# Optimization experiments

Measured on AMD Instinct MI355X. Metric: run time of the kernel, lower is better.

Reference implementation:

```python
import jax, jax.numpy as jnp
import numpy as np

SIGMA = 1.0
RADIUS = 3          # Gaussian kernel radius -> kernel size 7
TAU = 1.0
ITERATIONS = 20
EPS = 1e-6


def _gauss_kernel_1d(sigma: float, radius: int) -> jnp.ndarray:
    x = jnp.arange(-radius, radius + 1, dtype=jnp.float32)
    k = jnp.exp(-0.5 * (x / sigma) ** 2)
    return k / k.sum()


def _smooth(v: jnp.ndarray, k1d: jnp.ndarray) -> jnp.ndarray:
    """Separable Gaussian smoothing of a (1, C, D, H, W) field, 'same' padding."""
    C = v.shape[1]
    r = (k1d.size - 1) // 2
    for ax in range(3):
        shape = [1, 1, 1]
        shape[ax] = k1d.size
        ker = jnp.tile(k1d.reshape((1, 1) + tuple(shape)), (C, 1, 1, 1, 1))
        pad = [(r, r) if i == ax else (0, 0) for i in range(3)]
        v = jax.lax.conv_general_dilated(
            v, ker, window_strides=(1, 1, 1), padding=pad,
            dimension_numbers=('NCDHW', 'OIDHW', 'NCDHW'),
            feature_group_count=C)
    return v


def _warp(image: jnp.ndarray, disp: jnp.ndarray) -> jnp.ndarray:
    """Trilinear warp of (1,1,D,H,W) image by voxel displacement (1,3,D,H,W)."""
    D, H, W = image.shape[2:]
    gd, gh, gw = jnp.meshgrid(
        jnp.arange(D, dtype=disp.dtype),
        jnp.arange(H, dtype=disp.dtype),
        jnp.arange(W, dtype=disp.dtype), indexing='ij')
    coords = [gd + disp[0, 0], gh + disp[0, 1], gw + disp[0, 2]]
    warped = jax.scipy.ndimage.map_coordinates(image[0, 0], coords, order=1, mode='nearest')
    return warped[None, None]


def _spatial_gradient(img: jnp.ndarray) -> jnp.ndarray:
    # img: (D, H, W) -> (3, D, H, W), central differences
    return jnp.stack(jnp.gradient(img))


def _demon_forces_dual(warped, fixed, fixed_grad):
    # warped/fixed: (1,1,D,H,W); dual gradient = mean of moving/fixed gradients
    diff = (warped - fixed)[0, 0]                      # (D,H,W)
    g = 0.5 * (_spatial_gradient(warped[0, 0]) + fixed_grad)  # (3,D,H,W)
    denom = (g ** 2).sum(axis=0) + diff ** 2           # (D,H,W)
    f = jnp.where(denom > EPS, diff * g / denom, 0.0)  # (3,D,H,W)
    return f[None]                                     # (1,3,D,H,W)


def setup_inputs() -> dict:
    key = jax.random.key(0)
    k1, k2 = jax.random.split(key)
    shape = (1, 1, 128, 128, 128)
    moving_image = jax.random.uniform(k1, shape, dtype=jnp.float32)
    fixed_image = jax.random.uniform(k2, shape, dtype=jnp.float32)
    return {"moving_image": moving_image, "fixed_image": fixed_image}


def reference(moving_image, fixed_image):
    kernel = _gauss_kernel_1d(SIGMA, RADIUS)
    fixed_grad = _spatial_gradient(fixed_image[0, 0])
    vf0 = jnp.zeros((1, 3) + moving_image.shape[2:], dtype=moving_image.dtype)

    def step(vf, _):
        warped = _warp(moving_image, vf)
        forces = _demon_forces_dual(warped, fixed_image, fixed_grad)
        vf = _smooth(vf + TAU * forces, kernel)
        return vf, None

    vf, _ = jax.lax.scan(step, vf0, None, length=ITERATIONS)
    return vf
```

## Files before the change

kernel.cpp:

```cpp
#include <hip/hip_runtime.h>

static constexpr int DIM = 128;
static constexpr int N = DIM * DIM * DIM;
static constexpr int ITERS = 20;
static constexpr float EPS = 1e-6f;

#define W0 0.39905028f
#define W1 0.24203624f
#define W2 0.05400559f
#define W3 0.00443305f

__device__ __forceinline__ int clamp_i(int v, int lo, int hi) {
    return min(max(v, lo), hi);
}

#define ROWS 22
#define SC(c, r) ((((c) * ROWS) + (r)) << 7)

template <bool FIRST>
__global__ __launch_bounds__(256) void forces_xy_kernel(const float* __restrict__ wpd,
                                                        const float* __restrict__ fix,
                                                        const float* __restrict__ vf,
                                                        float* __restrict__ u2) {
    int b = blockIdx.x;
    int z = b & 127;
    int y0 = (b >> 7) << 4;

    __shared__ float S[3 * ROWS * 128];

    for (int e = threadIdx.x; e < ROWS * 32; e += 256) {
        int x4 = e & 31;
        int r  = e >> 5;
        int gy = y0 + r - 3;
        float4 rz = make_float4(0, 0, 0, 0);
        float4 ry = make_float4(0, 0, 0, 0);
        float4 rx = make_float4(0, 0, 0, 0);
        if (gy >= 0 && gy < 128) {
            int idx = (z << 14) + (gy << 7) + (x4 << 2);
            int xb = x4 << 2;

            float4 wc4 = *(const float4*)(wpd + idx);
            float4 fc4 = *(const float4*)(fix + idx);

            int iyp = (gy < 127) ? idx + 128   : idx;
            int iym = (gy > 0)   ? idx - 128   : idx;
            int izp = (z < 127)  ? idx + 16384 : idx;
            int izm = (z > 0)    ? idx - 16384 : idx;

            float4 wyp = *(const float4*)(wpd + iyp), wym = *(const float4*)(wpd + iym);
            float4 wzp = *(const float4*)(wpd + izp), wzm = *(const float4*)(wpd + izm);
            float4 fyp = *(const float4*)(fix + iyp), fym = *(const float4*)(fix + iym);
            float4 fzp = *(const float4*)(fix + izp), fzm = *(const float4*)(fix + izm);

            float wl = (xb > 0)   ? wpd[idx - 1] : 0.0f;
            float wr = (xb < 124) ? wpd[idx + 4] : 0.0f;
            float fl = (xb > 0)   ? fix[idx - 1] : 0.0f;
            float fr = (xb < 124) ? fix[idx + 4] : 0.0f;

            float wcv[4] = {wc4.x, wc4.y, wc4.z, wc4.w};
            float fcv[4] = {fc4.x, fc4.y, fc4.z, fc4.w};
            float wypv[4] = {wyp.x, wyp.y, wyp.z, wyp.w};
            float wymv[4] = {wym.x, wym.y, wym.z, wym.w};
            float wzpv[4] = {wzp.x, wzp.y, wzp.z, wzp.w};
            float wzmv[4] = {wzm.x, wzm.y, wzm.z, wzm.w};
            float fypv[4] = {fyp.x, fyp.y, fyp.z, fyp.w};
            float fymv[4] = {fym.x, fym.y, fym.z, fym.w};
            float fzpv[4] = {fzp.x, fzp.y, fzp.z, fzp.w};
            float fzmv[4] = {fzm.x, fzm.y, fzm.z, fzm.w};

            float4 vz4 = FIRST ? make_float4(0, 0, 0, 0) : *(const float4*)(vf + idx);
            float4 vy4 = FIRST ? make_float4(0, 0, 0, 0) : *(const float4*)(vf + N + idx);
            float4 vx4 = FIRST ? make_float4(0, 0, 0, 0) : *(const float4*)(vf + 2 * N + idx);
            float vzv[4] = {vz4.x, vz4.y, vz4.z, vz4.w};
            float vyv[4] = {vy4.x, vy4.y, vy4.z, vy4.w};
            float vxv[4] = {vx4.x, vx4.y, vx4.z, vx4.w};

            float ozv[4], oyv[4], oxv[4];
#pragma unroll
            for (int i = 0; i < 4; ++i) {
                float wc = wcv[i], fc = fcv[i];
                float diff = wc - fc;

                float gwz = (z == 0)   ? (wzpv[i] - wc)
                          : (z == 127) ? (wc - wzmv[i])
                          : 0.5f * (wzpv[i] - wzmv[i]);
                float gfz = (z == 0)   ? (fzpv[i] - fc)
                          : (z == 127) ? (fc - fzmv[i])
                          : 0.5f * (fzpv[i] - fzmv[i]);
                float grz = 0.5f * (gwz + gfz);

                float gwy = (gy == 0)   ? (wypv[i] - wc)
                          : (gy == 127) ? (wc - wymv[i])
                          : 0.5f * (wypv[i] - wymv[i]);
                float gfy = (gy == 0)   ? (fypv[i] - fc)
                          : (gy == 127) ? (fc - fymv[i])
                          : 0.5f * (fypv[i] - fymv[i]);
                float gry = 0.5f * (gwy + gfy);

                float wleft  = (i == 0) ? wl : wcv[i - 1];
                float wright = (i == 3) ? wr : wcv[i + 1];
                float fleft  = (i == 0) ? fl : fcv[i - 1];
                float fright = (i == 3) ? fr : fcv[i + 1];
                int xi = xb + i;
                float gwx = (xi == 0)   ? (wright - wc)
                          : (xi == 127) ? (wc - wleft)
                          : 0.5f * (wright - wleft);
                float gfx = (xi == 0)   ? (fright - fc)
                          : (xi == 127) ? (fc - fleft)
                          : 0.5f * (fright - fleft);
                float grx = 0.5f * (gwx + gfx);

                float denom = grz * grz + gry * gry + grx * grx + diff * diff;
                float s = (denom > EPS) ? (diff / denom) : 0.0f;
                ozv[i] = vzv[i] + s * grz;
                oyv[i] = vyv[i] + s * gry;
                oxv[i] = vxv[i] + s * grx;
            }
            rz = make_float4(ozv[0], ozv[1], ozv[2], ozv[3]);
            ry = make_float4(oyv[0], oyv[1], oyv[2], oyv[3]);
            rx = make_float4(oxv[0], oxv[1], oxv[2], oxv[3]);
        }
        *(float4*)(S + SC(0, r) + (x4 << 2)) = rz;
        *(float4*)(S + SC(1, r) + (x4 << 2)) = ry;
        *(float4*)(S + SC(2, r) + (x4 << 2)) = rx;
    }
    __syncthreads();

    float4 xb[3][3];
#pragma unroll
    for (int it = 0; it < 3; ++it) {
        int e = threadIdx.x + it * 256;
        if (e < ROWS * 32) {
            int x4 = e & 31;
            int r  = e >> 5;
#pragma unroll
            for (int c = 0; c < 3; ++c) {
                const float* base = S + SC(c, r) + (x4 << 2);
                float4 v0 = *(const float4*)base;
                float4 m1 = (x4 > 0)  ? *(const float4*)(base - 4) : make_float4(0, 0, 0, 0);
                float4 p1 = (x4 < 31) ? *(const float4*)(base + 4) : make_float4(0, 0, 0, 0);
                float w[12] = {m1.x, m1.y, m1.z, m1.w,
                               v0.x, v0.y, v0.z, v0.w,
                               p1.x, p1.y, p1.z, p1.w};
                float o[4];
#pragma unroll
                for (int i = 0; i < 4; ++i) {
                    o[i] = W3 * (w[i + 1] + w[i + 7]) + W2 * (w[i + 2] + w[i + 6])
                         + W1 * (w[i + 3] + w[i + 5]) + W0 * w[i + 4];
                }
                xb[it][c] = make_float4(o[0], o[1], o[2], o[3]);
            }
        }
    }
    __syncthreads();
#pragma unroll
    for (int it = 0; it < 3; ++it) {
        int e = threadIdx.x + it * 256;
        if (e < ROWS * 32) {
            int x4 = e & 31;
            int r  = e >> 5;
#pragma unroll
            for (int c = 0; c < 3; ++c)
                *(float4*)(S + SC(c, r) + (x4 << 2)) = xb[it][c];
        }
    }
    __syncthreads();

    for (int e = threadIdx.x; e < 16 * 32 * 3; e += 256) {
        int x4 = e & 31;
        int t2 = e >> 5;
        int y  = t2 & 15;
        int c  = t2 >> 4;
        const float* base = S + SC(c, y) + (x4 << 2);
        float4 v0 = *(const float4*)(base);
        float4 v1 = *(const float4*)(base + (1 << 7));
        float4 v2 = *(const float4*)(base + (2 << 7));
        float4 v3 = *(const float4*)(base + (3 << 7));
        float4 v4 = *(const float4*)(base + (4 << 7));
        float4 v5 = *(const float4*)(base + (5 << 7));
        float4 v6 = *(const float4*)(base + (6 << 7));
        float4 acc;
        acc.x = W3 * (v0.x + v6.x) + W2 * (v1.x + v5.x) + W1 * (v2.x + v4.x) + W0 * v3.x;
        acc.y = W3 * (v0.y + v6.y) + W2 * (v1.y + v5.y) + W1 * (v2.y + v4.y) + W0 * v3.y;
        acc.z = W3 * (v0.z + v6.z) + W2 * (v1.z + v5.z) + W1 * (v2.z + v4.z) + W0 * v3.z;
        acc.w = W3 * (v0.w + v6.w) + W2 * (v1.w + v5.w) + W1 * (v2.w + v4.w) + W0 * v3.w;
        *(float4*)(u2 + (size_t)c * N + ((size_t)z << 14) + ((y0 + y) << 7) + (x4 << 2)) = acc;
    }
}

template <bool DO_WARP>
__global__ __launch_bounds__(256) void zblur_warp_kernel(const float* __restrict__ u2,
                                                         const float* __restrict__ mov,
                                                         float* __restrict__ vf,
                                                         float* __restrict__ warped) {
    int g = blockIdx.x * 256 + threadIdx.x;
    int col = g & 16383;
    int zc  = g >> 14;
    int z0  = zc << 4;
    int x = col & 127, y = col >> 7;

    float bz[3][16];
#pragma unroll
    for (int c = 0; c < 3; ++c) {
        const float* inp = u2 + (size_t)c * N + col;
        float win[22];
#pragma unroll
        for (int i = 0; i < 22; ++i) {
            int zz = z0 - 3 + i;
            win[i] = (zz >= 0 && zz < 128) ? inp[(size_t)zz << 14] : 0.0f;
        }
#pragma unroll
        for (int k = 0; k < 16; ++k) {
            bz[c][k] = W3 * (win[k] + win[k + 6]) + W2 * (win[k + 1] + win[k + 5])
                     + W1 * (win[k + 2] + win[k + 4]) + W0 * win[k + 3];
        }
        float* outp = vf + (size_t)c * N + col;
#pragma unroll
        for (int k = 0; k < 16; ++k)
            outp[(size_t)(z0 + k) << 14] = bz[c][k];
    }

    if (DO_WARP) {
        for (int k = 0; k < 16; ++k) {
            int z = z0 + k;
            float cz = (float)z + bz[0][k];
            float cy = (float)y + bz[1][k];
            float cx = (float)x + bz[2][k];

            float flz = floorf(cz), fly = floorf(cy), flx = floorf(cx);
            float fz = cz - flz, fy = cy - fly, fx = cx - flx;

            int zi = (int)flz, yi = (int)fly, xi = (int)flx;
            int z0c = clamp_i(zi, 0, DIM - 1), z1c = clamp_i(zi + 1, 0, DIM - 1);
            int y0c = clamp_i(yi, 0, DIM - 1), y1c = clamp_i(yi + 1, 0, DIM - 1);
            int x0c = clamp_i(xi, 0, DIM - 1), x1c = clamp_i(xi + 1, 0, DIM - 1);

            int b00 = (z0c << 14) + (y0c << 7);
            int b01 = (z0c << 14) + (y1c << 7);
            int b10 = (z1c << 14) + (y0c << 7);
            int b11 = (z1c << 14) + (y1c << 7);

            float v000 = mov[b00 + x0c], v001 = mov[b00 + x1c];
            float v010 = mov[b01 + x0c], v011 = mov[b01 + x1c];
            float v100 = mov[b10 + x0c], v101 = mov[b10 + x1c];
            float v110 = mov[b11 + x0c], v111 = mov[b11 + x1c];

            float c00 = v000 + fx * (v001 - v000);
            float c01 = v010 + fx * (v011 - v010);
            float c10 = v100 + fx * (v101 - v100);
            float c11 = v110 + fx * (v111 - v110);
            float c0 = c00 + fy * (c01 - c00);
            float c1 = c10 + fy * (c11 - c10);
            warped[((size_t)z << 14) + col] = c0 + fz * (c1 - c0);
        }
    }
}

extern "C" void kernel_launch(void* const* d_in, const int* in_sizes, int n_in,
                              void* d_out, int out_size, void* d_ws, size_t ws_size,
                              hipStream_t stream) {
    const float* mov = (const float*)d_in[0];
    const float* fix = (const float*)d_in[1];
    float* vf = (float*)d_out;
    float* ws = (float*)d_ws;
    float* warped = ws;
    float* u2     = ws + (size_t)N;

    const int BLK = 256;
    const int gridFX = 128 * 8;
    const int gridZW = (N / 16) / BLK;

    forces_xy_kernel<true><<<gridFX, BLK, 0, stream>>>(mov, fix, nullptr, u2);
    zblur_warp_kernel<true><<<gridZW, BLK, 0, stream>>>(u2, mov, vf, warped);

    for (int it = 1; it < ITERS - 1; ++it) {
        forces_xy_kernel<false><<<gridFX, BLK, 0, stream>>>(warped, fix, vf, u2);
        zblur_warp_kernel<true><<<gridZW, BLK, 0, stream>>>(u2, mov, vf, warped);
    }
    forces_xy_kernel<false><<<gridFX, BLK, 0, stream>>>(warped, fix, vf, u2);
    zblur_warp_kernel<false><<<gridZW, BLK, 0, stream>>>(u2, mov, vf, warped);
}
```

Baseline: 887.7 us.

## Merge iteration kernels into one persistent cooperative kernel with grid syncs

Replaces the 40 alternating forces/xy-blur and z-blur/warp launches with a single cooperative persistent kernel that loops over iterations and uses grid.sync between phases. The z-blur chunk drops from 16 to 8 slices per thread so enough work items exist for the persistent grid. The x-blur in shared memory now runs one channel at a time with extra barriers to cut register pressure. Grid size comes from an occupancy query. This removes launch gaps but adds grid-wide barrier cost and more redundant z-halo loads.

```diff
diff --git a/kernel.cpp b/kernel.cpp
--- a/kernel.cpp
+++ b/kernel.cpp
@@ -1,4 +1,7 @@
 #include <hip/hip_runtime.h>
+#include <hip/hip_cooperative_groups.h>
+
+namespace cg = cooperative_groups;
 
 static constexpr int DIM = 128;
 static constexpr int N = DIM * DIM * DIM;
@@ -17,242 +20,248 @@
 #define ROWS 22
 #define SC(c, r) ((((c) * ROWS) + (r)) << 7)
 
-template <bool FIRST>
-__global__ __launch_bounds__(256) void forces_xy_kernel(const float* __restrict__ wpd,
-                                                        const float* __restrict__ fix,
-                                                        const float* __restrict__ vf,
-                                                        float* __restrict__ u2) {
-    int b = blockIdx.x;
-    int z = b & 127;
-    int y0 = (b >> 7) << 4;
-
+__global__ __launch_bounds__(256, 4) void varreg_persistent(
+        const float* __restrict__ mov, const float* __restrict__ fix,
+        float* __restrict__ vf, float* __restrict__ warped,
+        float* __restrict__ u2) {
+    cg::grid_group grid = cg::this_grid();
     __shared__ float S[3 * ROWS * 128];
-
-    for (int e = threadIdx.x; e < ROWS * 32; e += 256) {
-        int x4 = e & 31;
-        int r  = e >> 5;
-        int gy = y0 + r - 3;
-        float4 rz = make_float4(0, 0, 0, 0);
-        float4 ry = make_float4(0, 0, 0, 0);
-        float4 rx = make_float4(0, 0, 0, 0);
-        if (gy >= 0 && gy < 128) {
-            int idx = (z << 14) + (gy << 7) + (x4 << 2);
-            int xb = x4 << 2;
-
-            float4 wc4 = *(const float4*)(wpd + idx);
-            float4 fc4 = *(const float4*)(fix + idx);
-
-            int iyp = (gy < 127) ? idx + 128   : idx;
-            int iym = (gy > 0)   ? idx - 128   : idx;
-            int izp = (z < 127)  ? idx + 16384 : idx;
-            int izm = (z > 0)    ? idx - 16384 : idx;
-
-            float4 wyp = *(const float4*)(wpd + iyp), wym = *(const float4*)(wpd + iym);
-            float4 wzp = *(const float4*)(wpd + izp), wzm = *(const float4*)(wpd + izm);
-            float4 fyp = *(const float4*)(fix + iyp), fym = *(const float4*)(fix + iym);
-            float4 fzp = *(const float4*)(fix + izp), fzm = *(const float4*)(fix + izm);
-
-            float wl = (xb > 0)   ? wpd[idx - 1] : 0.0f;
-            float wr = (xb < 124) ? wpd[idx + 4] : 0.0f;
-            float fl = (xb > 0)   ? fix[idx - 1] : 0.0f;
-            float fr = (xb < 124) ? fix[idx + 4] : 0.0f;
-
-            float wcv[4] = {wc4.x, wc4.y, wc4.z, wc4.w};
-            float fcv[4] = {fc4.x, fc4.y, fc4.z, fc4.w};
-            float wypv[4] = {wyp.x, wyp.y, wyp.z, wyp.w};
-            float wymv[4] = {wym.x, wym.y, wym.z, wym.w};
-            float wzpv[4] = {wzp.x, wzp.y, wzp.z, wzp.w};
-            float wzmv[4] = {wzm.x, wzm.y, wzm.z, wzm.w};
-            float fypv[4] = {fyp.x, fyp.y, fyp.z, fyp.w};
-            float fymv[4] = {fym.x, fym.y, fym.z, fym.w};
-            float fzpv[4] = {fzp.x, fzp.y, fzp.z, fzp.w};
-            float fzmv[4] = {fzm.x, fzm.y, fzm.z, fzm.w};
-
-            float4 vz4 = FIRST ? make_float4(0, 0, 0, 0) : *(const float4*)(vf + idx);
-            float4 vy4 = FIRST ? make_float4(0, 0, 0, 0) : *(const float4*)(vf + N + idx);
-            float4 vx4 = FIRST ? make_float4(0, 0, 0, 0) : *(const float4*)(vf + 2 * N + idx);
-            float vzv[4] = {vz4.x, vz4.y, vz4.z, vz4.w};
-            float vyv[4] = {vy4.x, vy4.y, vy4.z, vy4.w};
-            float vxv[4] = {vx4.x, vx4.y, vx4.z, vx4.w};
-
-            float ozv[4], oyv[4], oxv[4];
-#pragma unroll
-            for (int i = 0; i < 4; ++i) {
-                float wc = wcv[i], fc = fcv[i];
-                float diff = wc - fc;
-
-                float gwz = (z == 0)   ? (wzpv[i] - wc)
-                          : (z == 127) ? (wc - wzmv[i])
-                          : 0.5f * (wzpv[i] - wzmv[i]);
-                float gfz = (z == 0)   ? (fzpv[i] - fc)
-                          : (z == 127) ? (fc - fzmv[i])
-                          : 0.5f * (fzpv[i] - fzmv[i]);
-                float grz = 0.5f * (gwz + gfz);
-
-                float gwy = (gy == 0)   ? (wypv[i] - wc)
-                          : (gy == 127) ? (wc - wymv[i])
-                          : 0.5f * (wypv[i] - wymv[i]);
-                float gfy = (gy == 0)   ? (fypv[i] - fc)
-                          : (gy == 127) ? (fc - fymv[i])
-                          : 0.5f * (fypv[i] - fymv[i]);
-                float gry = 0.5f * (gwy + gfy);
-
-                float wleft  = (i == 0) ? wl : wcv[i - 1];
-                float wright = (i == 3) ? wr : wcv[i + 1];
-                float fleft  = (i == 0) ? fl : fcv[i - 1];
-                float fright = (i == 3) ? fr : fcv[i + 1];
-                int xi = xb + i;
-                float gwx = (xi == 0)   ? (wright - wc)
-                          : (xi == 127) ? (wc - wleft)
-                          : 0.5f * (wright - wleft);
-                float gfx = (xi == 0)   ? (fright - fc)
-                          : (xi == 127) ? (fc - fleft)
-                          : 0.5f * (fright - fleft);
-                float grx = 0.5f * (gwx + gfx);
-
-                float denom = grz * grz + gry * gry + grx * grx + diff * diff;
-                float s = (denom > EPS) ? (diff / denom) : 0.0f;
-                ozv[i] = vzv[i] + s * grz;
-                oyv[i] = vyv[i] + s * gry;
-                oxv[i] = vxv[i] + s * grx;
-            }
-            rz = make_float4(ozv[0], ozv[1], ozv[2], ozv[3]);
-            ry = make_float4(oyv[0], oyv[1], oyv[2], oyv[3]);
-            rx = make_float4(oxv[0], oxv[1], oxv[2], oxv[3]);
+    const int tid = threadIdx.x;
+
+    for (int iter = 0; iter < ITERS; ++iter) {
+        const bool first = (iter == 0);
+        const float* wpd = first ? mov : warped;
+
+        for (int tile = blockIdx.x; tile < 1024; tile += gridDim.x) {
+            int z = tile & 127;
+            int y0 = (tile >> 7) << 4;
+
+            for (int e = tid; e < ROWS * 32; e += 256) {
+                int x4 = e & 31;
+                int r  = e >> 5;
+                int gy = y0 + r - 3;
+                float4 rz = make_float4(0, 0, 0, 0);
+                float4 ry = make_float4(0, 0, 0, 0);
+                float4 rx = make_float4(0, 0, 0, 0);
+                if (gy >= 0 && gy < 128) {
+                    int idx = (z << 14) + (gy << 7) + (x4 << 2);
+                    int xb = x4 << 2;
+
+                    float4 wc4 = *(const float4*)(wpd + idx);
+                    float4 fc4 = *(const float4*)(fix + idx);
+
+                    int iyp = (gy < 127) ? idx + 128   : idx;
+                    int iym = (gy > 0)   ? idx - 128   : idx;
+                    int izp = (z < 127)  ? idx + 16384 : idx;
+                    int izm = (z > 0)    ? idx - 16384 : idx;
+
+                    float4 wyp = *(const float4*)(wpd + iyp), wym = *(const float4*)(wpd + iym);
+                    float4 wzp = *(const float4*)(wpd + izp), wzm = *(const float4*)(wpd + izm);
+                    float4 fyp = *(const float4*)(fix + iyp), fym = *(const float4*)(fix + iym);
+                    float4 fzp = *(const float4*)(fix + izp), fzm = *(const float4*)(fix + izm);
+
+                    float wl = (xb > 0)   ? wpd[idx - 1] : 0.0f;
+                    float wr = (xb < 124) ? wpd[idx + 4] : 0.0f;
+                    float fl = (xb > 0)   ? fix[idx - 1] : 0.0f;
+                    float fr = (xb < 124) ? fix[idx + 4] : 0.0f;
+
+                    float wcv[4] = {wc4.x, wc4.y, wc4.z, wc4.w};
+                    float fcv[4] = {fc4.x, fc4.y, fc4.z, fc4.w};
+                    float wypv[4] = {wyp.x, wyp.y, wyp.z, wyp.w};
+                    float wymv[4] = {wym.x, wym.y, wym.z, wym.w};
+                    float wzpv[4] = {wzp.x, wzp.y, wzp.z, wzp.w};
+                    float wzmv[4] = {wzm.x, wzm.y, wzm.z, wzm.w};
+                    float fypv[4] = {fyp.x, fyp.y, fyp.z, fyp.w};
+                    float fymv[4] = {fym.x, fym.y, fym.z, fym.w};
+                    float fzpv[4] = {fzp.x, fzp.y, fzp.z, fzp.w};
+                    float fzmv[4] = {fzm.x, fzm.y, fzm.z, fzm.w};
+
+                    float4 vz4 = first ? make_float4(0, 0, 0, 0) : *(const float4*)(vf + idx);
+                    float4 vy4 = first ? make_float4(0, 0, 0, 0) : *(const float4*)(vf + N + idx);
+                    float4 vx4 = first ? make_float4(0, 0, 0, 0) : *(const float4*)(vf + 2 * N + idx);
+                    float vzv[4] = {vz4.x, vz4.y, vz4.z, vz4.w};
+                    float vyv[4] = {vy4.x, vy4.y, vy4.z, vy4.w};
+                    float vxv[4] = {vx4.x, vx4.y, vx4.z, vx4.w};
+
+                    float ozv[4], oyv[4], oxv[4];
+#pragma unroll
+                    for (int i = 0; i < 4; ++i) {
+                        float wc = wcv[i], fc = fcv[i];
+                        float diff = wc - fc;
+
+                        float gwz = (z == 0)   ? (wzpv[i] - wc)
+                                  : (z == 127) ? (wc - wzmv[i])
+                                  : 0.5f * (wzpv[i] - wzmv[i]);
+                        float gfz = (z == 0)   ? (fzpv[i] - fc)
+                                  : (z == 127) ? (fc - fzmv[i])
+                                  : 0.5f * (fzpv[i] - fzmv[i]);
+                        float grz = 0.5f * (gwz + gfz);
+
+                        float gwy = (gy == 0)   ? (wypv[i] - wc)
+                                  : (gy == 127) ? (wc - wymv[i])
+                                  : 0.5f * (wypv[i] - wymv[i]);
+                        float gfy = (gy == 0)   ? (fypv[i] - fc)
+                                  : (gy == 127) ? (fc - fymv[i])
+                                  : 0.5f * (fypv[i] - fymv[i]);
+                        float gry = 0.5f * (gwy + gfy);
+
+                        float wleft  = (i == 0) ? wl : wcv[i - 1];
+                        float wright = (i == 3) ? wr : wcv[i + 1];
+                        float fleft  = (i == 0) ? fl : fcv[i - 1];
+                        float fright = (i == 3) ? fr : fcv[i + 1];
+                        int xi = xb + i;
+                        float gwx = (xi == 0)   ? (wright - wc)
+                                  : (xi == 127) ? (wc - wleft)
+                                  : 0.5f * (wright - wleft);
+                        float gfx = (xi == 0)   ? (fright - fc)
+                                  : (xi == 127) ? (fc - fleft)
+                                  : 0.5f * (fright - fleft);
+                        float grx = 0.5f * (gwx + gfx);
+
+                        float denom = grz * grz + gry * gry + grx * grx + diff * diff;
+                        float s = (denom > EPS) ? (diff / denom) : 0.0f;
+                        ozv[i] = vzv[i] + s * grz;
+                        oyv[i] = vyv[i] + s * gry;
+                        oxv[i] = vxv[i] + s * grx;
+                    }
+                    rz = make_float4(ozv[0], ozv[1], ozv[2], ozv[3]);
+                    ry = make_float4(oyv[0], oyv[1], oyv[2], oyv[3]);
+                    rx = make_float4(oxv[0], oxv[1], oxv[2], oxv[3]);
+                }
+                *(float4*)(S + SC(0, r) + (x4 << 2)) = rz;
+                *(float4*)(S + SC(1, r) + (x4 << 2)) = ry;
+                *(float4*)(S + SC(2, r) + (x4 << 2)) = rx;
+            }
+            __syncthreads();
+
+#pragma unroll
+            for (int c = 0; c < 3; ++c) {
+                float4 xbv[3];
+#pragma unroll
+                for (int it2 = 0; it2 < 3; ++it2) {
+                    int e = tid + it2 * 256;
+                    if (e < ROWS * 32) {
+                        int x4 = e & 31;
+                        int r  = e >> 5;
+                        const float* base = S + SC(c, r) + (x4 << 2);
+                        float4 v0 = *(const float4*)base;
+                        float4 m1 = (x4 > 0)  ? *(const float4*)(base - 4) : make_float4(0, 0, 0, 0);
+                        float4 p1 = (x4 < 31) ? *(const float4*)(base + 4) : make_float4(0, 0, 0, 0);
+                        float w[12] = {m1.x, m1.y, m1.z, m1.w,
+                                       v0.x, v0.y, v0.z, v0.w,
+                                       p1.x, p1.y, p1.z, p1.w};
+                        float o[4];
+#pragma unroll
+                        for (int i = 0; i < 4; ++i) {
+                            o[i] = W3 * (w[i + 1] + w[i + 7]) + W2 * (w[i + 2] + w[i + 6])
+                                 + W1 * (w[i + 3] + w[i + 5]) + W0 * w[i + 4];
+                        }
+                        xbv[it2] = make_float4(o[0], o[1], o[2], o[3]);
+                    }
+                }
+                __syncthreads();
+#pragma unroll
+                for (int it2 = 0; it2 < 3; ++it2) {
+                    int e = tid + it2 * 256;
+                    if (e < ROWS * 32) {
+                        int x4 = e & 31;
+                        int r  = e >> 5;
+                        *(float4*)(S + SC(c, r) + (x4 << 2)) = xbv[it2];
+                    }
+                }
+                __syncthreads();
+            }
+
+            for (int e = tid; e < 16 * 32 * 3; e += 256) {
+                int x4 = e & 31;
+                int t2 = e >> 5;
+                int y  = t2 & 15;
+                int c  = t2 >> 4;
+                const float* base = S + SC(c, y) + (x4 << 2);
+                float4 v0 = *(const float4*)(base);
+                float4 v1 = *(const float4*)(base + (1 << 7));
+                float4 v2 = *(const float4*)(base + (2 << 7));
+                float4 v3 = *(const float4*)(base + (3 << 7));
+                float4 v4 = *(const float4*)(base + (4 << 7));
+                float4 v5 = *(const float4*)(base + (5 << 7));
+                float4 v6 = *(const float4*)(base + (6 << 7));
+                float4 acc;
+                acc.x = W3 * (v0.x + v6.x) + W2 * (v1.x + v5.x) + W1 * (v2.x + v4.x) + W0 * v3.x;
+                acc.y = W3 * (v0.y + v6.y) + W2 * (v1.y + v5.y) + W1 * (v2.y + v4.y) + W0 * v3.y;
+                acc.z = W3 * (v0.z + v6.z) + W2 * (v1.z + v5.z) + W1 * (v2.z + v4.z) + W0 * v3.z;
+                acc.w = W3 * (v0.w + v6.w) + W2 * (v1.w + v5.w) + W1 * (v2.w + v4.w) + W0 * v3.w;
+                *(float4*)(u2 + (size_t)c * N + ((size_t)z << 14) + ((y0 + y) << 7) + (x4 << 2)) = acc;
+            }
+            __syncthreads();
         }
-        *(float4*)(S + SC(0, r) + (x4 << 2)) = rz;
-        *(float4*)(S + SC(1, r) + (x4 << 2)) = ry;
-        *(float4*)(S + SC(2, r) + (x4 << 2)) = rx;
-    }
-    __syncthreads();
-
-    float4 xb[3][3];
-#pragma unroll
-    for (int it = 0; it < 3; ++it) {
-        int e = threadIdx.x + it * 256;
-        if (e < ROWS * 32) {
-            int x4 = e & 31;
-            int r  = e >> 5;
+
+        grid.sync();
+
+        const bool do_warp = (iter < ITERS - 1);
+        for (int g = blockIdx.x * 256 + tid; g < 262144; g += gridDim.x * 256) {
+            int col = g & 16383;
+            int zc  = g >> 14;
+            int z0  = zc << 3;
+            int x = col & 127, y = col >> 7;
+
+            float bz[3][8];
 #pragma unroll
             for (int c = 0; c < 3; ++c) {
-                const float* base = S + SC(c, r) + (x4 << 2);
-                float4 v0 = *(const float4*)base;
-                float4 m1 = (x4 > 0)  ? *(const float4*)(base - 4) : make_float4(0, 0, 0, 0);
-                float4 p1 = (x4 < 31) ? *(const float4*)(base + 4) : make_float4(0, 0, 0, 0);
-                float w[12] = {m1.x, m1.y, m1.z, m1.w,
-                               v0.x, v0.y, v0.z, v0.w,
-                               p1.x, p1.y, p1.z, p1.w};
-                float o[4];
-#pragma unroll
-                for (int i = 0; i < 4; ++i) {
-                    o[i] = W3 * (w[i + 1] + w[i + 7]) + W2 * (w[i + 2] + w[i + 6])
-                         + W1 * (w[i + 3] + w[i + 5]) + W0 * w[i + 4];
-                }
-                xb[it][c] = make_float4(o[0], o[1], o[2], o[3]);
+                const float* inp = u2 + (size_t)c * N + col;
+                float win[14];
+#pragma unroll
+                for (int i = 0; i < 14; ++i) {
+                    int zz = z0 - 3 + i;
+                    win[i] = (zz >= 0 && zz < 128) ? inp[(size_t)zz << 14] : 0.0f;
+                }
+#pragma unroll
+                for (int k = 0; k < 8; ++k) {
+                    bz[c][k] = W3 * (win[k] + win[k + 6]) + W2 * (win[k + 1] + win[k + 5])
+                             + W1 * (win[k + 2] + win[k + 4]) + W0 * win[k + 3];
+                }
+                float* outp = vf + (size_t)c * N + col;
+#pragma unroll
+                for (int k = 0; k < 8; ++k)
+                    outp[(size_t)(z0 + k) << 14] = bz[c][k];
+            }
+
+            if (do_warp) {
+                for (int k = 0; k < 8; ++k) {
+                    int z = z0 + k;
+                    float cz = (float)z + bz[0][k];
+                    float cy = (float)y + bz[1][k];
+                    float cx = (float)x + bz[2][k];
+
+                    float flz = floorf(cz), fly = floorf(cy), flx = floorf(cx);
+                    float fz = cz - flz, fy = cy - fly, fx = cx - flx;
+
+                    int zi = (int)flz, yi = (int)fly, xi = (int)flx;
+                    int z0c = clamp_i(zi, 0, DIM - 1), z1c = clamp_i(zi + 1, 0, DIM - 1);
+                    int y0c = clamp_i(yi, 0, DIM - 1), y1c = clamp_i(yi + 1, 0, DIM - 1);
+                    int x0c = clamp_i(xi, 0, DIM - 1), x1c = clamp_i(xi + 1, 0, DIM - 1);
+
+                    int b00 = (z0c << 14) + (y0c << 7);
+                    int b01 = (z0c << 14) + (y1c << 7);
+                    int b10 = (z1c << 14) + (y0c << 7);
+                    int b11 = (z1c << 14) + (y1c << 7);
+
+                    float v000 = mov[b00 + x0c], v001 = mov[b00 + x1c];
+                    float v010 = mov[b01 + x0c], v011 = mov[b01 + x1c];
+                    float v100 = mov[b10 + x0c], v101 = mov[b10 + x1c];
+                    float v110 = mov[b11 + x0c], v111 = mov[b11 + x1c];
+
+                    float c00 = v000 + fx * (v001 - v000);
+                    float c01 = v010 + fx * (v011 - v010);
+                    float c10 = v100 + fx * (v101 - v100);
+                    float c11 = v110 + fx * (v111 - v110);
+                    float c0 = c00 + fy * (c01 - c00);
+                    float c1 = c10 + fy * (c11 - c10);
+                    warped[((size_t)z << 14) + col] = c0 + fz * (c1 - c0);
+                }
             }
         }
-    }
-    __syncthreads();
-#pragma unroll
-    for (int it = 0; it < 3; ++it) {
-        int e = threadIdx.x + it * 256;
-        if (e < ROWS * 32) {
-            int x4 = e & 31;
-            int r  = e >> 5;
-#pragma unroll
-            for (int c = 0; c < 3; ++c)
-                *(float4*)(S + SC(c, r) + (x4 << 2)) = xb[it][c];
-        }
-    }
-    __syncthreads();
-
-    for (int e = threadIdx.x; e < 16 * 32 * 3; e += 256) {
-        int x4 = e & 31;
-        int t2 = e >> 5;
-        int y  = t2 & 15;
-        int c  = t2 >> 4;
-        const float* base = S + SC(c, y) + (x4 << 2);
-        float4 v0 = *(const float4*)(base);
-        float4 v1 = *(const float4*)(base + (1 << 7));
-        float4 v2 = *(const float4*)(base + (2 << 7));
-        float4 v3 = *(const float4*)(base + (3 << 7));
-        float4 v4 = *(const float4*)(base + (4 << 7));
-        float4 v5 = *(const float4*)(base + (5 << 7));
-        float4 v6 = *(const float4*)(base + (6 << 7));
-        float4 acc;
-        acc.x = W3 * (v0.x + v6.x) + W2 * (v1.x + v5.x) + W1 * (v2.x + v4.x) + W0 * v3.x;
-        acc.y = W3 * (v0.y + v6.y) + W2 * (v1.y + v5.y) + W1 * (v2.y + v4.y) + W0 * v3.y;
-        acc.z = W3 * (v0.z + v6.z) + W2 * (v1.z + v5.z) + W1 * (v2.z + v4.z) + W0 * v3.z;
-        acc.w = W3 * (v0.w + v6.w) + W2 * (v1.w + v5.w) + W1 * (v2.w + v4.w) + W0 * v3.w;
-        *(float4*)(u2 + (size_t)c * N + ((size_t)z << 14) + ((y0 + y) << 7) + (x4 << 2)) = acc;
-    }
-}
-
-template <bool DO_WARP>
-__global__ __launch_bounds__(256) void zblur_warp_kernel(const float* __restrict__ u2,
-                                                         const float* __restrict__ mov,
-                                                         float* __restrict__ vf,
-                                                         float* __restrict__ warped) {
-    int g = blockIdx.x * 256 + threadIdx.x;
-    int col = g & 16383;
-    int zc  = g >> 14;
-    int z0  = zc << 4;
-    int x = col & 127, y = col >> 7;
-
-    float bz[3][16];
-#pragma unroll
-    for (int c = 0; c < 3; ++c) {
-        const float* inp = u2 + (size_t)c * N + col;
-        float win[22];
-#pragma unroll
-        for (int i = 0; i < 22; ++i) {
-            int zz = z0 - 3 + i;
-            win[i] = (zz >= 0 && zz < 128) ? inp[(size_t)zz << 14] : 0.0f;
-        }
-#pragma unroll
-        for (int k = 0; k < 16; ++k) {
-            bz[c][k] = W3 * (win[k] + win[k + 6]) + W2 * (win[k + 1] + win[k + 5])
-                     + W1 * (win[k + 2] + win[k + 4]) + W0 * win[k + 3];
-        }
-        float* outp = vf + (size_t)c * N + col;
-#pragma unroll
-        for (int k = 0; k < 16; ++k)
-            outp[(size_t)(z0 + k) << 14] = bz[c][k];
-    }
-
-    if (DO_WARP) {
-        for (int k = 0; k < 16; ++k) {
-            int z = z0 + k;
-            float cz = (float)z + bz[0][k];
-            float cy = (float)y + bz[1][k];
-            float cx = (float)x + bz[2][k];
-
-            float flz = floorf(cz), fly = floorf(cy), flx = floorf(cx);
-            float fz = cz - flz, fy = cy - fly, fx = cx - flx;
-
-            int zi = (int)flz, yi = (int)fly, xi = (int)flx;
-            int z0c = clamp_i(zi, 0, DIM - 1), z1c = clamp_i(zi + 1, 0, DIM - 1);
-            int y0c = clamp_i(yi, 0, DIM - 1), y1c = clamp_i(yi + 1, 0, DIM - 1);
-            int x0c = clamp_i(xi, 0, DIM - 1), x1c = clamp_i(xi + 1, 0, DIM - 1);
-
-            int b00 = (z0c << 14) + (y0c << 7);
-            int b01 = (z0c << 14) + (y1c << 7);
-            int b10 = (z1c << 14) + (y0c << 7);
-            int b11 = (z1c << 14) + (y1c << 7);
-
-            float v000 = mov[b00 + x0c], v001 = mov[b00 + x1c];
-            float v010 = mov[b01 + x0c], v011 = mov[b01 + x1c];
-            float v100 = mov[b10 + x0c], v101 = mov[b10 + x1c];
-            float v110 = mov[b11 + x0c], v111 = mov[b11 + x1c];
-
-            float c00 = v000 + fx * (v001 - v000);
-            float c01 = v010 + fx * (v011 - v010);
-            float c10 = v100 + fx * (v101 - v100);
-            float c11 = v110 + fx * (v111 - v110);
-            float c0 = c00 + fy * (c01 - c00);
-            float c1 = c10 + fy * (c11 - c10);
-            warped[((size_t)z << 14) + col] = c0 + fz * (c1 - c0);
-        }
+
+        grid.sync();
     }
 }
 
@@ -266,17 +275,14 @@
     float* warped = ws;
     float* u2     = ws + (size_t)N;
 
-    const int BLK = 256;
-    const int gridFX = 128 * 8;
-    const int gridZW = (N / 16) / BLK;
-
-    forces_xy_kernel<true><<<gridFX, BLK, 0, stream>>>(mov, fix, nullptr, u2);
-    zblur_warp_kernel<true><<<gridZW, BLK, 0, stream>>>(u2, mov, vf, warped);
-
-    for (int it = 1; it < ITERS - 1; ++it) {
-        forces_xy_kernel<false><<<gridFX, BLK, 0, stream>>>(warped, fix, vf, u2);
-        zblur_warp_kernel<true><<<gridZW, BLK, 0, stream>>>(u2, mov, vf, warped);
-    }
-    forces_xy_kernel<false><<<gridFX, BLK, 0, stream>>>(warped, fix, vf, u2);
-    zblur_warp_kernel<false><<<gridZW, BLK, 0, stream>>>(u2, mov, vf, warped);
+    int maxBlocksPerCU = 0;
+    hipOccupancyMaxActiveBlocksPerMultiprocessor(&maxBlocksPerCU,
+        (const void*)varreg_persistent, 256, 0);
+    if (maxBlocksPerCU < 1) maxBlocksPerCU = 1;
+    int grid = maxBlocksPerCU * 256;
+    if (grid > 1024) grid = 1024;
+
+    void* args[] = {(void*)&mov, (void*)&fix, (void*)&vf, (void*)&warped, (void*)&u2};
+    hipLaunchCooperativeKernel((const void*)varreg_persistent,
+                               dim3(grid), dim3(256), args, 0, stream);
 }
```

After: 3.154 ms. +255.3%, slower.
